# Performance work log

Measured on AMD Instinct MI355X. Metric: run time of the kernel, lower is better.

Reference implementation:

```python
import jax, jax.numpy as jnp
import numpy as np

B, S, D = 2, 2048, 1024
H, DK, DV = 16, 64, 64


def setup_inputs() -> dict:
    key = jax.random.key(0)
    ks = jax.random.split(key, 9)
    s = 0.02
    return {
        "x": jax.random.normal(ks[0], (B, S, D), dtype=jnp.float32),
        "mask": jnp.zeros((B, S), dtype=bool),  # True = padded position
        "Wq": jax.random.normal(ks[1], (D, H * DK), dtype=jnp.float32) * s,
        "bq": jnp.zeros((H * DK,), dtype=jnp.float32),
        "Wk": jax.random.normal(ks[2], (D, H * DK), dtype=jnp.float32) * s,
        "bk": jnp.zeros((H * DK,), dtype=jnp.float32),
        "Wv": jax.random.normal(ks[3], (D, H * DV), dtype=jnp.float32) * s,
        "bv": jnp.zeros((H * DV,), dtype=jnp.float32),
        "Wo": jax.random.normal(ks[4], (H * DV, D), dtype=jnp.float32) * s,
        "bo": jnp.zeros((D,), dtype=jnp.float32),
    }


def reference(x, mask, Wq, bq, Wk, bk, Wv, bv, Wo, bo):
    Bx, Sx, _ = x.shape
    # projections -> [B, H, S, dk/dv]
    q = (x @ Wq + bq).reshape(Bx, Sx, H, DK).transpose(0, 2, 1, 3)
    k = (x @ Wk + bk).reshape(Bx, Sx, H, DK).transpose(0, 2, 1, 3)
    v = (x @ Wv + bv).reshape(Bx, Sx, H, DV).transpose(0, 2, 1, 3)
    # scaled QK^T: [B, H, Sq, Sk]
    scores = jnp.einsum("bhqd,bhkd->bhqk", q, k) / jnp.sqrt(jnp.float32(DK))
    neg_inf = jnp.float32(-jnp.inf)
    # padding mask: True masks out key positions
    scores = jnp.where(mask[:, None, None, :], neg_inf, scores)
    # causal mask
    causal = jnp.triu(jnp.ones((Sx, Sx), dtype=bool), k=1)
    scores = jnp.where(causal[None, None, :, :], neg_inf, scores)
    attn = jax.nn.softmax(scores, axis=-1)
    out = jnp.einsum("bhqk,bhkd->bhqd", attn, v)  # [B, H, S, dv]
    out = out.transpose(0, 2, 1, 3).reshape(Bx, Sx, H * DV)
    return out @ Wo + bo
```

## Files before the change

kernel.cpp:

```cpp
#include <hip/hip_runtime.h>
#include <stdint.h>

typedef __bf16 bf16_t;
typedef __bf16 bf16x8 __attribute__((ext_vector_type(8)));
typedef float f32x4 __attribute__((ext_vector_type(4)));

#define S_LEN 2048
#define D_MODEL 1024
#define NH 16
#define DKV 64
#define BATCH 2

#define QSCALE 0.1803368801111204f

__device__ __forceinline__ uint16_t f2bfu(float f) {
    union { float f; uint32_t u; } c; c.f = f;
    return (uint16_t)((c.u + 0x7fffu + ((c.u >> 16) & 1u)) >> 16);
}
__device__ __forceinline__ bf16_t f2bf(float f) {
    union { uint16_t s; bf16_t b; } o; o.s = f2bfu(f);
    return o.b;
}
__device__ __forceinline__ uint32_t pack2t(float lo, float hi) {
    union { float f; uint32_t u; } a, b; a.f = lo; b.f = hi;
    return __builtin_amdgcn_perm(b.u, a.u, 0x07060302);
}
__device__ __forceinline__ void gld_lds16(const bf16_t* g, bf16_t* l) {
    __builtin_amdgcn_global_load_lds(
        (const __attribute__((address_space(1))) void*)g,
        (__attribute__((address_space(3))) void*)l, 16, 0, 0);
}

__global__ __launch_bounds__(256) void k_convert_x(const float* __restrict__ x,
                                                   bf16_t* __restrict__ xb, int n) {
    int i = (blockIdx.x * 256 + threadIdx.x) * 4;
    if (i < n) {
        float4 v = *(const float4*)(x + i);
        xb[i + 0] = f2bf(v.x);
        xb[i + 1] = f2bf(v.y);
        xb[i + 2] = f2bf(v.z);
        xb[i + 3] = f2bf(v.w);
    }
}

__global__ __launch_bounds__(256) void k_transpose4(
    const float* __restrict__ Wq, const float* __restrict__ Wk,
    const float* __restrict__ Wv, const float* __restrict__ Wo,
    bf16_t* __restrict__ WqkvT, bf16_t* __restrict__ WoT) {
    __shared__ float tile[64][65];
    int k0 = blockIdx.x * 64;
    int n0 = blockIdx.y * 64;
    const float* W; bf16_t* WT; int np, nw;
    if (n0 < 3072) {
        W = (n0 < 1024) ? Wq : (n0 < 2048) ? Wk : Wv;
        np = n0 & 1023; WT = WqkvT; nw = n0;
    } else {
        W = Wo; np = n0 - 3072; WT = WoT; nw = n0 - 3072;
    }
    int tx = threadIdx.x & 63, ty = threadIdx.x >> 6;
    #pragma unroll
    for (int r = ty; r < 64; r += 4)
        tile[r][tx] = W[(size_t)(k0 + r) * 1024 + np + tx];
    __syncthreads();
    #pragma unroll
    for (int r = ty; r < 64; r += 4)
        WT[(size_t)(nw + r) * 1024 + k0 + tx] = f2bf(tile[tx][r]);
}

#define BM 128
#define BN 128
#define BKK 64

__global__ __launch_bounds__(256) void k_gemm_qkv(
    const bf16_t* __restrict__ A, const bf16_t* __restrict__ BT, int K,
    const float* __restrict__ bias0, const float* __restrict__ bias1,
    const float* __restrict__ bias2,
    bf16_t* __restrict__ outQ, bf16_t* __restrict__ outK, bf16_t* __restrict__ outVt) {
    __shared__ __align__(16) bf16_t As[BM * BKK];
    __shared__ __align__(16) bf16_t Bs[BN * BKK];
    int m0 = blockIdx.x * BM;
    int n0 = blockIdx.y * BN;
    int t = threadIdx.x;
    int wid = t >> 6, lane = t & 63, l15 = lane & 15, quad = lane >> 4;
    int wr = (wid >> 1) * 64, wc = (wid & 1) * 64;
    int srow = t >> 3;
    int schunk = (t & 7) ^ (srow & 7);
    int sldst = (t & 7) * 8;
    const f32x4 fzero = {0.f, 0.f, 0.f, 0.f};
    f32x4 acc[4][4];
    #pragma unroll
    for (int i = 0; i < 4; i++)
        #pragma unroll
        for (int j = 0; j < 4; j++) acc[i][j] = fzero;

    int r7 = l15 & 7;
    for (int k0 = 0; k0 < K; k0 += BKK) {
        #pragma unroll
        for (int p = 0; p < 4; p++) {
            int r = p * 32 + srow;
            gld_lds16(&A[(size_t)(m0 + r) * K + k0 + schunk * 8], &As[r * 64 + sldst]);
            gld_lds16(&BT[(size_t)(n0 + r) * K + k0 + schunk * 8], &Bs[r * 64 + sldst]);
        }
        __syncthreads();
        #pragma unroll
        for (int kk = 0; kk < BKK; kk += 32) {
            int g = quad + (kk >> 3);
            int col = ((g ^ r7) << 3);
            bf16x8 af[4], bfr[4];
            #pragma unroll
            for (int mt = 0; mt < 4; mt++)
                af[mt] = *(const bf16x8*)&As[(wr + mt * 16 + l15) * 64 + col];
            #pragma unroll
            for (int nt = 0; nt < 4; nt++)
                bfr[nt] = *(const bf16x8*)&Bs[(wc + nt * 16 + l15) * 64 + col];
            #pragma unroll
            for (int mt = 0; mt < 4; mt++)
                #pragma unroll
                for (int nt = 0; nt < 4; nt++)
                    acc[mt][nt] = __builtin_amdgcn_mfma_f32_16x16x32_bf16(
                        af[mt], bfr[nt], acc[mt][nt], 0, 0, 0);
        }
        __syncthreads();
    }

    #pragma unroll
    for (int mt = 0; mt < 4; mt++) {
        #pragma unroll
        for (int nt = 0; nt < 4; nt++) {
            int gc = n0 + wc + nt * 16 + l15;
            int sec = gc >> 10;
            int nn = gc & 1023;
            int h = nn >> 6, d = nn & 63;
            int gr0 = m0 + wr + mt * 16 + quad * 4;
            int b = gr0 >> 11, s0 = gr0 & 2047;
            if (sec == 2) {
                float bv = bias2[nn];
                uint2 pk;
                pk.x = pack2t(acc[mt][nt][0] + bv, acc[mt][nt][1] + bv);
                pk.y = pack2t(acc[mt][nt][2] + bv, acc[mt][nt][3] + bv);
                *(uint2*)&outVt[(((size_t)(b * NH + h)) * DKV + d) * S_LEN + s0] = pk;
            } else {
                const float* bias = (sec == 0) ? bias0 : bias1;
                float bv = bias[nn];
                #pragma unroll
                for (int r = 0; r < 4; r++) {
                    float val = acc[mt][nt][r] + bv;
                    size_t idx = (((size_t)(b * NH + h)) * S_LEN + s0 + r) * DKV + d;
                    if (sec == 0) outQ[idx] = f2bf(val * QSCALE);
                    else          outK[idx] = f2bf(val);
                }
            }
        }
    }
}

__global__ __launch_bounds__(256) void k_gemm_out(
    const bf16_t* __restrict__ A, const bf16_t* __restrict__ BT, int N, int K,
    const float* __restrict__ bias, float* __restrict__ outF) {
    __shared__ __align__(16) bf16_t As[128 * 64];
    __shared__ __align__(16) bf16_t Bs[64 * 64];
    int m0 = blockIdx.x * 128;
    int n0 = blockIdx.y * 64;
    int t = threadIdx.x;
    int wid = t >> 6, lane = t & 63, l15 = lane & 15, quad = lane >> 4;
    int wr = wid * 32;
    int srow = t >> 3;
    int schunk = (t & 7) ^ (srow & 7);
    int sldst = (t & 7) * 8;
    const f32x4 fzero = {0.f, 0.f, 0.f, 0.f};
    f32x4 acc[2][4];
    #pragma unroll
    for (int i = 0; i < 2; i++)
        #pragma unroll
        for (int j = 0; j < 4; j++) acc[i][j] = fzero;

    int r7 = l15 & 7;
    for (int k0 = 0; k0 < K; k0 += 64) {
        #pragma unroll
        for (int p = 0; p < 4; p++) {
            int r = p * 32 + srow;
            gld_lds16(&A[(size_t)(m0 + r) * K + k0 + schunk * 8], &As[r * 64 + sldst]);
        }
        #pragma unroll
        for (int p = 0; p < 2; p++) {
            int r = p * 32 + srow;
            gld_lds16(&BT[(size_t)(n0 + r) * K + k0 + schunk * 8], &Bs[r * 64 + sldst]);
        }
        __syncthreads();
        #pragma unroll
        for (int kk = 0; kk < 64; kk += 32) {
            int g = quad + (kk >> 3);
            int col = ((g ^ r7) << 3);
            bf16x8 af[2], bfr[4];
            #pragma unroll
            for (int mt = 0; mt < 2; mt++)
                af[mt] = *(const bf16x8*)&As[(wr + mt * 16 + l15) * 64 + col];
            #pragma unroll
            for (int nt = 0; nt < 4; nt++)
                bfr[nt] = *(const bf16x8*)&Bs[(nt * 16 + l15) * 64 + col];
            #pragma unroll
            for (int mt = 0; mt < 2; mt++)
                #pragma unroll
                for (int nt = 0; nt < 4; nt++)
                    acc[mt][nt] = __builtin_amdgcn_mfma_f32_16x16x32_bf16(
                        af[mt], bfr[nt], acc[mt][nt], 0, 0, 0);
        }
        __syncthreads();
    }

    #pragma unroll
    for (int mt = 0; mt < 2; mt++) {
        #pragma unroll
        for (int nt = 0; nt < 4; nt++) {
            #pragma unroll
            for (int r = 0; r < 4; r++) {
                int gr = m0 + wr + mt * 16 + quad * 4 + r;
                int gc = n0 + nt * 16 + l15;
                outF[(size_t)gr * N + gc] = acc[mt][nt][r] + bias[gc];
            }
        }
    }
}

__global__ __launch_bounds__(256) void k_attn8(
    const bf16_t* __restrict__ Q, const bf16_t* __restrict__ Kg,
    const bf16_t* __restrict__ Vt, const unsigned char* __restrict__ mask,
    bf16_t* __restrict__ O) {
    __shared__ __align__(16) bf16_t QPs[64 * 64];
    __shared__ __align__(16) bf16_t Ks[128 * 64];
    __shared__ __align__(16) bf16_t Vs[64 * 128];

    int bid = blockIdx.x;
    int bh = bid & 31;
    int u = bid >> 5;
    int a = u & 7, g2 = u >> 3;
    int qt = (g2 == 0) ? 31 - a : (g2 == 1) ? a : (g2 == 2) ? 23 - a : 8 + a;
    int b = bh >> 4, h = bh & 15;
    int t = threadIdx.x;
    int w = t >> 6, lane = t & 63, l15 = lane & 15, quad = lane >> 4;
    int r7 = l15 & 7;

    const bf16_t* Qbase = Q + ((size_t)bh * S_LEN + qt * 64) * DKV;
    {
        int r = t >> 3, c8 = t & 7;
        int sc = (c8 ^ (r & 7)) * 8;
        *(uint4*)&QPs[r * 64 + sc]        = *(const uint4*)&Qbase[(size_t)r * 64 + c8 * 8];
        *(uint4*)&QPs[(r + 32) * 64 + sc] = *(const uint4*)&Qbase[(size_t)(r + 32) * 64 + c8 * 8];
    }
    __syncthreads();
    bf16x8 qf0 = *(const bf16x8*)&QPs[(w * 16 + l15) * 64 + ((quad ^ r7) << 3)];
    bf16x8 qf1 = *(const bf16x8*)&QPs[(w * 16 + l15) * 64 + (((4 + quad) ^ r7) << 3)];

    const f32x4 fzero = {0.f, 0.f, 0.f, 0.f};
    f32x4 oacc[4];
    f32x4 lacc = fzero;
    #pragma unroll
    for (int nt = 0; nt < 4; nt++) oacc[nt] = fzero;

    const bf16_t one_b = (bf16_t)1.0f;
    const bf16x8 onesf = {one_b, one_b, one_b, one_b, one_b, one_b, one_b, one_b};

    int qg   = qt * 64 + w * 16 + l15;
    int qmin = qt * 64 + w * 16;
    int qmax = qmin + 15;
    int ktmax = qt >> 1;

    int srK = t >> 3;
    int scK = (t & 7) ^ (srK & 7);
    int slK = (t & 7) * 8;
    int srV = t >> 4;
    int scV = (t & 15) ^ (srV & 7);
    int slV = (t & 15) * 8;

    for (int kt = 0; kt <= ktmax; kt++) {
        __syncthreads();
        {
            const bf16_t* Kb = Kg + ((size_t)bh * S_LEN + kt * 128) * DKV;
            #pragma unroll
            for (int p = 0; p < 4; p++) {
                int r = p * 32 + srK;
                gld_lds16(&Kb[(size_t)r * 64 + scK * 8], &Ks[r * 64 + slK]);
            }
            #pragma unroll
            for (int p = 0; p < 4; p++) {
                int r = p * 16 + srV;
                gld_lds16(&Vt[((size_t)bh * DKV + r) * S_LEN + kt * 128 + scV * 8],
                          &Vs[r * 128 + slV]);
            }
        }
        __syncthreads();

        #pragma unroll
        for (int sub = 0; sub < 2; sub++) {
            int kbase = kt * 128 + sub * 64;
            if (kbase > qmax) break;

            uint32_t mb[4];
            #pragma unroll
            for (int mt = 0; mt < 4; mt++)
                mb[mt] = *(const uint32_t*)&mask[b * S_LEN + kbase + mt * 16 + quad * 4];

            f32x4 sacc[4];
            #pragma unroll
            for (int mt = 0; mt < 4; mt++) sacc[mt] = fzero;
            #pragma unroll
            for (int kk = 0; kk < 64; kk += 32) {
                bf16x8 qf = kk ? qf1 : qf0;
                int col = (((quad + (kk >> 3)) ^ r7) << 3);
                #pragma unroll
                for (int mt = 0; mt < 4; mt++) {
                    bf16x8 af = *(const bf16x8*)&Ks[(sub * 64 + mt * 16 + l15) * 64 + col];
                    sacc[mt] = __builtin_amdgcn_mfma_f32_16x16x32_bf16(af, qf, sacc[mt], 0, 0, 0);
                }
            }

            bool diag = (kbase + 63 > qmin);
            #pragma unroll
            for (int mt = 0; mt < 4; mt++) {
                #pragma unroll
                for (int r = 0; r < 4; r++)
                    sacc[mt][r] += (float)((mb[mt] >> (8 * r)) & 0xffu) * -1e30f;
                if (diag) {
                    int kgb = kbase + mt * 16 + quad * 4;
                    #pragma unroll
                    for (int r = 0; r < 4; r++)
                        if (kgb + r > qg) sacc[mt][r] = -1e30f;
                }
            }
            #pragma unroll
            for (int mt = 0; mt < 4; mt++) {
                uint2 pk;
                pk.x = pack2t(exp2f(sacc[mt][0]), exp2f(sacc[mt][1]));
                pk.y = pack2t(exp2f(sacc[mt][2]), exp2f(sacc[mt][3]));
                int pc = (mt * 2 + (quad >> 1)) ^ r7;
                *(uint2*)&QPs[(w * 16 + l15) * 64 + pc * 8 + (quad & 1) * 4] = pk;
            }

            #pragma unroll
            for (int kk = 0; kk < 64; kk += 32) {
                bf16x8 pf = *(const bf16x8*)&QPs[(w * 16 + l15) * 64 +
                                                 (((quad + (kk >> 3)) ^ r7) << 3)];
                int g2v = sub * 8 + (kk >> 3) + quad;
                int vcol = ((g2v ^ r7) << 3);
                #pragma unroll
                for (int nt = 0; nt < 4; nt++) {
                    bf16x8 vf = *(const bf16x8*)&Vs[(nt * 16 + l15) * 128 + vcol];
                    oacc[nt] = __builtin_amdgcn_mfma_f32_16x16x32_bf16(pf, vf, oacc[nt], 0, 0, 0);
                }
                lacc = __builtin_amdgcn_mfma_f32_16x16x32_bf16(pf, onesf, lacc, 0, 0, 0);
            }
        }
    }

    #pragma unroll
    for (int r = 0; r < 4; r++) {
        float l = lacc[r];
        float invl = l > 0.f ? 1.f / l : 0.f;
        int q = qt * 64 + w * 16 + quad * 4 + r;
        #pragma unroll
        for (int nt = 0; nt < 4; nt++) {
            int d = nt * 16 + l15;
            O[((size_t)b * S_LEN + q) * D_MODEL + h * DKV + d] = f2bf(oacc[nt][r] * invl);
        }
    }
}

extern "C" void kernel_launch(void* const* d_in, const int* in_sizes, int n_in,
                              void* d_out, int out_size, void* d_ws, size_t ws_size,
                              hipStream_t stream) {
    const float* x = (const float*)d_in[0];
    const unsigned char* mask = (const unsigned char*)d_in[1];
    const float* Wq = (const float*)d_in[2];
    const float* bq = (const float*)d_in[3];
    const float* Wk = (const float*)d_in[4];
    const float* bk = (const float*)d_in[5];
    const float* Wv = (const float*)d_in[6];
    const float* bv = (const float*)d_in[7];
    const float* Wo = (const float*)d_in[8];
    const float* bo = (const float*)d_in[9];
    float* out = (float*)d_out;

    char* ws = (char*)d_ws;
    const size_t MB = 1024 * 1024;
    bf16_t* xb    = (bf16_t*)(ws + 0 * MB);
    bf16_t* WqkvT = (bf16_t*)(ws + 8 * MB);
    bf16_t* WoT   = (bf16_t*)(ws + 14 * MB);
    bf16_t* Qb    = (bf16_t*)(ws + 16 * MB);
    bf16_t* Kb    = (bf16_t*)(ws + 24 * MB);
    bf16_t* Vtb   = (bf16_t*)(ws + 32 * MB);
    bf16_t* AOb   = (bf16_t*)(ws + 40 * MB);

    k_convert_x<<<dim3(4096), dim3(256), 0, stream>>>(x, xb, 4 * 1024 * 1024);
    k_transpose4<<<dim3(16, 64), dim3(256), 0, stream>>>(Wq, Wk, Wv, Wo, WqkvT, WoT);
    k_gemm_qkv<<<dim3(32, 24), dim3(256), 0, stream>>>(
        xb, WqkvT, 1024, bq, bk, bv, Qb, Kb, Vtb);
    k_attn8<<<dim3(1024), dim3(256), 0, stream>>>(Qb, Kb, Vtb, mask, AOb);
    k_gemm_out<<<dim3(32, 16), dim3(256), 0, stream>>>(
        AOb, WoT, 1024, 1024, bo, out);
}
```

Baseline: 191.6 us.

## Load K/V fragments directly from global memory in attention, drop LDS staging

The attention kernel no longer stages K and V tiles in shared memory with block-wide barriers. Each wave now reads its MFMA operand fragments for Q, K and V straight from global memory, relying on L2/L1 since the four waves share the same K/V. It also skips the padding-mask add when a wave-wide check finds no masked positions, raises wave priority around the MFMA groups, and sets launch bounds to 4 blocks per CU. Removing the barriers and most of the LDS use should raise occupancy and let waves run independently, at the cost of redundant global and cache traffic and unswizzled strided loads.

Result: slower. 268.3 us (+40.0%).

```diff
diff --git a/kernel.cpp b/kernel.cpp
--- a/kernel.cpp
+++ b/kernel.cpp
@@ -222,13 +222,11 @@
     }
 }
 
-__global__ __launch_bounds__(256) void k_attn8(
+__global__ __launch_bounds__(256, 4) void k_attn9(
     const bf16_t* __restrict__ Q, const bf16_t* __restrict__ Kg,
     const bf16_t* __restrict__ Vt, const unsigned char* __restrict__ mask,
     bf16_t* __restrict__ O) {
-    __shared__ __align__(16) bf16_t QPs[64 * 64];
-    __shared__ __align__(16) bf16_t Ks[128 * 64];
-    __shared__ __align__(16) bf16_t Vs[64 * 128];
+    __shared__ __align__(16) bf16_t Ps[64 * 64];
 
     int bid = blockIdx.x;
     int bh = bid & 31;
@@ -240,16 +238,23 @@
     int w = t >> 6, lane = t & 63, l15 = lane & 15, quad = lane >> 4;
     int r7 = l15 & 7;
 
-    const bf16_t* Qbase = Q + ((size_t)bh * S_LEN + qt * 64) * DKV;
+    bool maskany;
     {
-        int r = t >> 3, c8 = t & 7;
-        int sc = (c8 ^ (r & 7)) * 8;
-        *(uint4*)&QPs[r * 64 + sc]        = *(const uint4*)&Qbase[(size_t)r * 64 + c8 * 8];
-        *(uint4*)&QPs[(r + 32) * 64 + sc] = *(const uint4*)&Qbase[(size_t)(r + 32) * 64 + c8 * 8];
-    }
-    __syncthreads();
-    bf16x8 qf0 = *(const bf16x8*)&QPs[(w * 16 + l15) * 64 + ((quad ^ r7) << 3)];
-    bf16x8 qf1 = *(const bf16x8*)&QPs[(w * 16 + l15) * 64 + (((4 + quad) ^ r7) << 3)];
+        const uint2* mrow = (const uint2*)&mask[b * S_LEN];
+        uint2 m0 = mrow[lane], m1 = mrow[lane + 64];
+        uint2 m2 = mrow[lane + 128], m3 = mrow[lane + 192];
+        uint32_t mo = (m0.x | m0.y) | (m1.x | m1.y) | (m2.x | m2.y) | (m3.x | m3.y);
+        maskany = __any(mo != 0);
+    }
+
+    const bf16_t* Qrow = Q + ((size_t)bh * S_LEN + qt * 64 + w * 16 + l15) * DKV;
+    bf16x8 qf0 = *(const bf16x8*)&Qrow[quad * 8];
+    bf16x8 qf1 = *(const bf16x8*)&Qrow[32 + quad * 8];
+
+    const bf16_t* Kbh = Kg + (size_t)bh * S_LEN * DKV;
+    const bf16_t* Vbh = Vt + (size_t)bh * DKV * S_LEN;
+    const bf16_t* Kl = Kbh + l15 * DKV + quad * 8;
+    const bf16_t* Vl = Vbh + (size_t)l15 * S_LEN + quad * 8;
 
     const f32x4 fzero = {0.f, 0.f, 0.f, 0.f};
     f32x4 oacc[4];
@@ -265,62 +270,43 @@
     int qmax = qmin + 15;
     int ktmax = qt >> 1;
 
-    int srK = t >> 3;
-    int scK = (t & 7) ^ (srK & 7);
-    int slK = (t & 7) * 8;
-    int srV = t >> 4;
-    int scV = (t & 15) ^ (srV & 7);
-    int slV = (t & 15) * 8;
-
     for (int kt = 0; kt <= ktmax; kt++) {
-        __syncthreads();
-        {
-            const bf16_t* Kb = Kg + ((size_t)bh * S_LEN + kt * 128) * DKV;
-            #pragma unroll
-            for (int p = 0; p < 4; p++) {
-                int r = p * 32 + srK;
-                gld_lds16(&Kb[(size_t)r * 64 + scK * 8], &Ks[r * 64 + slK]);
-            }
-            #pragma unroll
-            for (int p = 0; p < 4; p++) {
-                int r = p * 16 + srV;
-                gld_lds16(&Vt[((size_t)bh * DKV + r) * S_LEN + kt * 128 + scV * 8],
-                          &Vs[r * 128 + slV]);
-            }
-        }
-        __syncthreads();
-
         #pragma unroll
         for (int sub = 0; sub < 2; sub++) {
             int kbase = kt * 128 + sub * 64;
             if (kbase > qmax) break;
 
-            uint32_t mb[4];
-            #pragma unroll
-            for (int mt = 0; mt < 4; mt++)
-                mb[mt] = *(const uint32_t*)&mask[b * S_LEN + kbase + mt * 16 + quad * 4];
-
             f32x4 sacc[4];
             #pragma unroll
             for (int mt = 0; mt < 4; mt++) sacc[mt] = fzero;
             #pragma unroll
             for (int kk = 0; kk < 64; kk += 32) {
                 bf16x8 qf = kk ? qf1 : qf0;
-                int col = (((quad + (kk >> 3)) ^ r7) << 3);
+                bf16x8 af[4];
+                #pragma unroll
+                for (int mt = 0; mt < 4; mt++)
+                    af[mt] = *(const bf16x8*)&Kl[(size_t)(kbase + mt * 16) * DKV + kk];
+                __builtin_amdgcn_s_setprio(1);
+                #pragma unroll
+                for (int mt = 0; mt < 4; mt++)
+                    sacc[mt] = __builtin_amdgcn_mfma_f32_16x16x32_bf16(
+                        af[mt], qf, sacc[mt], 0, 0, 0);
+                __builtin_amdgcn_s_setprio(0);
+            }
+
+            if (maskany) {
                 #pragma unroll
                 for (int mt = 0; mt < 4; mt++) {
-                    bf16x8 af = *(const bf16x8*)&Ks[(sub * 64 + mt * 16 + l15) * 64 + col];
-                    sacc[mt] = __builtin_amdgcn_mfma_f32_16x16x32_bf16(af, qf, sacc[mt], 0, 0, 0);
+                    uint32_t mb = *(const uint32_t*)&mask[b * S_LEN + kbase + mt * 16 + quad * 4];
+                    #pragma unroll
+                    for (int r = 0; r < 4; r++)
+                        sacc[mt][r] += (float)((mb >> (8 * r)) & 0xffu) * -1e30f;
                 }
             }
-
             bool diag = (kbase + 63 > qmin);
-            #pragma unroll
-            for (int mt = 0; mt < 4; mt++) {
-                #pragma unroll
-                for (int r = 0; r < 4; r++)
-                    sacc[mt][r] += (float)((mb[mt] >> (8 * r)) & 0xffu) * -1e30f;
-                if (diag) {
+            if (diag) {
+                #pragma unroll
+                for (int mt = 0; mt < 4; mt++) {
                     int kgb = kbase + mt * 16 + quad * 4;
                     #pragma unroll
                     for (int r = 0; r < 4; r++)
@@ -333,21 +319,24 @@
                 pk.x = pack2t(exp2f(sacc[mt][0]), exp2f(sacc[mt][1]));
                 pk.y = pack2t(exp2f(sacc[mt][2]), exp2f(sacc[mt][3]));
                 int pc = (mt * 2 + (quad >> 1)) ^ r7;
-                *(uint2*)&QPs[(w * 16 + l15) * 64 + pc * 8 + (quad & 1) * 4] = pk;
+                *(uint2*)&Ps[(w * 16 + l15) * 64 + pc * 8 + (quad & 1) * 4] = pk;
             }
 
             #pragma unroll
             for (int kk = 0; kk < 64; kk += 32) {
-                bf16x8 pf = *(const bf16x8*)&QPs[(w * 16 + l15) * 64 +
+                bf16x8 pf = *(const bf16x8*)&Ps[(w * 16 + l15) * 64 +
                                                  (((quad + (kk >> 3)) ^ r7) << 3)];
-                int g2v = sub * 8 + (kk >> 3) + quad;
-                int vcol = ((g2v ^ r7) << 3);
-                #pragma unroll
-                for (int nt = 0; nt < 4; nt++) {
-                    bf16x8 vf = *(const bf16x8*)&Vs[(nt * 16 + l15) * 128 + vcol];
-                    oacc[nt] = __builtin_amdgcn_mfma_f32_16x16x32_bf16(pf, vf, oacc[nt], 0, 0, 0);
-                }
+                bf16x8 vf[4];
+                #pragma unroll
+                for (int nt = 0; nt < 4; nt++)
+                    vf[nt] = *(const bf16x8*)&Vl[(size_t)(nt * 16) * S_LEN + kbase + kk];
+                __builtin_amdgcn_s_setprio(1);
+                #pragma unroll
+                for (int nt = 0; nt < 4; nt++)
+                    oacc[nt] = __builtin_amdgcn_mfma_f32_16x16x32_bf16(
+                        pf, vf[nt], oacc[nt], 0, 0, 0);
                 lacc = __builtin_amdgcn_mfma_f32_16x16x32_bf16(pf, onesf, lacc, 0, 0, 0);
+                __builtin_amdgcn_s_setprio(0);
             }
         }
     }
@@ -394,7 +383,7 @@
     k_transpose4<<<dim3(16, 64), dim3(256), 0, stream>>>(Wq, Wk, Wv, Wo, WqkvT, WoT);
     k_gemm_qkv<<<dim3(32, 24), dim3(256), 0, stream>>>(
         xb, WqkvT, 1024, bq, bk, bv, Qb, Kb, Vtb);
-    k_attn8<<<dim3(1024), dim3(256), 0, stream>>>(Qb, Kb, Vtb, mask, AOb);
+    k_attn9<<<dim3(1024), dim3(256), 0, stream>>>(Qb, Kb, Vtb, mask, AOb);
     k_gemm_out<<<dim3(32, 16), dim3(256), 0, stream>>>(
         AOb, WoT, 1024, 1024, bo, out);
 }
```
